# Optimization experiments

Measured on AMD Instinct MI355X. Metric: run time of the kernel, lower is better.

The kernel has to match this reference:

```python
import jax, jax.numpy as jnp
import numpy as np

B, L, D, H = 2, 2048, 1024, 16
DK = D // H


def setup_inputs() -> dict:
    key = jax.random.key(0)
    ks = jax.random.split(key, 11)
    s = 1.0 / np.sqrt(D)
    inp = {
        "context_sequence": jax.random.normal(ks[0], (B, L, D), jnp.float32),
        "value_sequence": jax.random.normal(ks[1], (B, L, D), jnp.float32),
        "mask": jnp.tril(jnp.ones((L, L), jnp.int32)),  # causal mask [L, L]
        "Wq": jax.random.normal(ks[2], (D, D), jnp.float32) * s,
        "bq": jax.random.normal(ks[3], (D,), jnp.float32) * s,
        "Wk": jax.random.normal(ks[4], (D, D), jnp.float32) * s,
        "bk": jax.random.normal(ks[5], (D,), jnp.float32) * s,
        "Wv": jax.random.normal(ks[6], (D, D), jnp.float32) * s,
        "bv": jax.random.normal(ks[7], (D,), jnp.float32) * s,
        "Wo": jax.random.normal(ks[8], (D, D), jnp.float32) * s,
        "bo": jax.random.normal(ks[9], (D,), jnp.float32) * s,
    }
    return inp


def reference(context_sequence, value_sequence, mask, Wq, bq, Wk, bk, Wv, bv, Wo, bo):
    orig_dtype = context_sequence.dtype
    # QKV projections; Q,K from context, V from value stream
    Q = (context_sequence @ Wq + bq).reshape(B, L, H, DK)
    K = (context_sequence @ Wk + bk).reshape(B, L, H, DK)
    V = (value_sequence @ Wv + bv).reshape(B, L, H, DK)
    # fp32 QK^T with 1/sqrt(d_k) scaling -> [B, H, L, L]
    scores = jnp.einsum("bqhd,bkhd->bhqk", Q.astype(jnp.float32), K.astype(jnp.float32)) / jnp.sqrt(
        jnp.asarray(DK, jnp.float32)
    )
    # dtype-dependent neg fill (fp32 -> -inf); causal rows always have >=1 valid entry
    neg_fill = jnp.asarray(-jnp.inf, jnp.float32)
    scores = jnp.where(mask[None, None, :, :] == 0, neg_fill, scores)
    scores = scores.astype(orig_dtype)
    attn = jax.nn.softmax(scores, axis=-1)
    # dropout is identity in eval mode
    out = jnp.einsum("bhqk,bkhd->bqhd", attn, V).reshape(B, L, D)
    return out @ Wo + bo
```

## Files before the change

### kernel.cpp

```cpp
#include <hip/hip_runtime.h>
#include <hip/hip_bf16.h>
#include <stdint.h>

#define B_   2
#define L_   2048
#define D_   1024
#define H_   16
#define DK_  64

typedef __attribute__((ext_vector_type(4))) float f32x4;
typedef __attribute__((ext_vector_type(8))) short short8;
typedef unsigned short ushort_t;

__device__ __forceinline__ ushort_t f2bf(float f) {
    union { float f; uint32_t u; } v; v.f = f;
    uint32_t r = v.u + 0x7FFFu + ((v.u >> 16) & 1u);
    return (ushort_t)(r >> 16);
}
__device__ __forceinline__ float bf2f(ushort_t u) {
    union { uint32_t u; float f; } v; v.u = (uint32_t)u << 16; return v.f;
}

__device__ __forceinline__ void async_copy16(void* lds, const void* g) {
    __builtin_amdgcn_global_load_lds(
        (const __attribute__((address_space(1))) uint32_t*)g,
        (__attribute__((address_space(3))) uint32_t*)lds, 16, 0, 0);
}

__global__ void cast_f32_bf16(const float* __restrict__ s0, const float* __restrict__ s1,
                              ushort_t* __restrict__ d0, ushort_t* __restrict__ d1) {
    const float* s = blockIdx.z ? s1 : s0;
    ushort_t*    d = blockIdx.z ? d1 : d0;
    int i = (blockIdx.x * 256 + threadIdx.x) * 4;
    float4 v = *(const float4*)(s + i);
    ushort4 o;
    o.x = f2bf(v.x); o.y = f2bf(v.y); o.z = f2bf(v.z); o.w = f2bf(v.w);
    *(ushort4*)(d + i) = o;
}

__global__ void transpose_w(const float* __restrict__ w0, const float* __restrict__ w1,
                            const float* __restrict__ w2, const float* __restrict__ w3,
                            ushort_t* __restrict__ out) {
    __shared__ float tile[32][33];
    const float* w = (blockIdx.z == 0) ? w0 : (blockIdx.z == 1) ? w1 : (blockIdx.z == 2) ? w2 : w3;
    ushort_t* o = out + (size_t)blockIdx.z * D_ * D_;
    int tx = threadIdx.x, ty = threadIdx.y;
    int k0 = blockIdx.y * 32, d0 = blockIdx.x * 32;
#pragma unroll
    for (int i = 0; i < 4; i++)
        tile[ty + i * 8][tx] = w[(size_t)(k0 + ty + i * 8) * D_ + d0 + tx];
    __syncthreads();
#pragma unroll
    for (int i = 0; i < 4; i++)
        o[(size_t)(d0 + ty + i * 8) * D_ + k0 + tx] = f2bf(tile[tx][ty + i * 8]);
}

__device__ __forceinline__ void gemm_main(const ushort_t* __restrict__ A,
                                          const ushort_t* __restrict__ WT,
                                          char* smem, int m0, int n0, int tid,
                                          f32x4 (&acc)[4][4]) {
    const int wid = tid >> 6, lane = tid & 63;
    const int wm = (wid >> 1) * 64, wn = (wid & 1) * 64;
#pragma unroll
    for (int i = 0; i < 4; i++)
#pragma unroll
        for (int j = 0; j < 4; j++) { f32x4 z = {0.f, 0.f, 0.f, 0.f}; acc[i][j] = z; }

    auto stage = [&](int buf, int k0) {
        char* bA = smem + buf * 32768;
        char* bB = bA + 16384;
#pragma unroll
        for (int i = 0; i < 4; i++) {
            int flat = i * 256 + tid; int row = flat >> 3; int win = (flat & 7) * 16;
            const char* srcA = (const char*)A + ((size_t)(m0 + row) * D_ + k0) * 2 + (win ^ ((row & 7) << 4));
            async_copy16(bA + (i * 256 + wid * 64) * 16, srcA);
            const char* srcB = (const char*)WT + ((size_t)(n0 + row) * D_ + k0) * 2 + (win ^ ((row & 7) << 4));
            async_copy16(bB + (i * 256 + wid * 64) * 16, srcB);
        }
    };

    stage(0, 0);
    int cur = 0;
    for (int k0 = 0; k0 < D_; k0 += 64) {
        __syncthreads();
        if (k0 + 64 < D_) stage(cur ^ 1, k0 + 64);
        const char* bA = smem + cur * 32768;
        const char* bB = bA + 16384;
#pragma unroll
        for (int ks = 0; ks < 2; ks++) {
            short8 af[4], bf[4];
            int kb = ks * 64 + ((lane >> 4) << 4);
#pragma unroll
            for (int t = 0; t < 4; t++) {
                int ml = wm + t * 16 + (lane & 15);
                af[t] = *(const short8*)(bA + ml * 128 + (kb ^ ((ml & 7) << 4)));
                int nl = wn + t * 16 + (lane & 15);
                bf[t] = *(const short8*)(bB + nl * 128 + (kb ^ ((nl & 7) << 4)));
            }
#pragma unroll
            for (int mt = 0; mt < 4; mt++)
#pragma unroll
                for (int nt = 0; nt < 4; nt++)
                    acc[mt][nt] = __builtin_amdgcn_mfma_f32_16x16x32_bf16(af[mt], bf[nt], acc[mt][nt], 0, 0, 0);
        }
        cur ^= 1;
    }
}

#define QSCALE 0.18033688f

__global__ __launch_bounds__(256, 2) void gemm_qkv(
    const ushort_t* __restrict__ Xc, const ushort_t* __restrict__ Xv,
    const ushort_t* __restrict__ WT0,
    const float* __restrict__ bq, const float* __restrict__ bk, const float* __restrict__ bv,
    ushort_t* __restrict__ qw, ushort_t* __restrict__ kw, ushort_t* __restrict__ vtw) {
    __shared__ __align__(16) char smem[65536];
    const int z = blockIdx.z;
    const ushort_t* A  = (z == 2) ? Xv : Xc;
    const ushort_t* WT = WT0 + (size_t)z * D_ * D_;
    const float* bias  = (z == 0) ? bq : (z == 1) ? bk : bv;
    const int tid = threadIdx.x, wid = tid >> 6, lane = tid & 63;
    const int m0 = blockIdx.y * 128, n0 = blockIdx.x * 128;
    const int wm = (wid >> 1) * 64, wn = (wid & 1) * 64;
    f32x4 acc[4][4];
    gemm_main(A, WT, smem, m0, n0, tid, acc);
#pragma unroll
    for (int mt = 0; mt < 4; mt++)
#pragma unroll
        for (int nt = 0; nt < 4; nt++)
#pragma unroll
            for (int r = 0; r < 4; r++) {
                int m = m0 + wm + mt * 16 + ((lane >> 4) << 2) + r;
                int n = n0 + wn + nt * 16 + (lane & 15);
                float v = acc[mt][nt][r] + bias[n];
                int b = m >> 11, tok = m & 2047, h = n >> 6, dk = n & 63;
                if (z == 0)      qw[((size_t)(b * H_ + h) * L_ + tok) * DK_ + dk] = f2bf(v * QSCALE);
                else if (z == 1) kw[((size_t)(b * H_ + h) * L_ + tok) * DK_ + dk] = f2bf(v);
                else             vtw[((size_t)(b * H_ + h) * DK_ + dk) * L_ + tok] = f2bf(v);
            }
}

__global__ __launch_bounds__(256, 2) void gemm_out(
    const ushort_t* __restrict__ O, const ushort_t* __restrict__ WT,
    const float* __restrict__ bo, float* __restrict__ out) {
    __shared__ __align__(16) char smem[65536];
    const int tid = threadIdx.x, wid = tid >> 6, lane = tid & 63;
    const int m0 = blockIdx.y * 128, n0 = blockIdx.x * 128;
    const int wm = (wid >> 1) * 64, wn = (wid & 1) * 64;
    f32x4 acc[4][4];
    gemm_main(O, WT, smem, m0, n0, tid, acc);
#pragma unroll
    for (int mt = 0; mt < 4; mt++)
#pragma unroll
        for (int nt = 0; nt < 4; nt++)
#pragma unroll
            for (int r = 0; r < 4; r++) {
                int m = m0 + wm + mt * 16 + ((lane >> 4) << 2) + r;
                int n = n0 + wn + nt * 16 + (lane & 15);
                out[(size_t)m * D_ + n] = acc[mt][nt][r] + bo[n];
            }
}

__global__ __launch_bounds__(256, 2) void attn_kernel(
    const ushort_t* __restrict__ qws, const ushort_t* __restrict__ kws,
    const ushort_t* __restrict__ vtws, ushort_t* __restrict__ ows) {
    __shared__ __align__(16) char smem[37888];
    const int tid = threadIdx.x, wid = tid >> 6, lane = tid & 63;
    const int lo = lane & 15, hi = lane >> 4;
    const int bid = blockIdx.x;
    const int xcd = bid & 7, slot = bid >> 3;
    const int bh = xcd * 4 + (slot >> 4);
    const int pi = slot & 15;
    char*  Pw = smem + wid * 9216;
    float* lw = (float*)(smem + 36864) + wid * 64;

    short8 ones;
#pragma unroll
    for (int i = 0; i < 8; i++) ones[i] = (short)0x3F80;

#pragma unroll 1
    for (int half = 0; half < 2; half++) {
        const int qtb = half ? (31 - pi) : pi;
        const int Q0 = qtb * 64;

        short8 qf[4][2];
#pragma unroll
        for (int qt = 0; qt < 4; qt++)
#pragma unroll
            for (int ks = 0; ks < 2; ks++)
                qf[qt][ks] = *(const short8*)(qws + (size_t)(bh * L_ + Q0 + qt * 16 + lo) * DK_ + ks * 32 + hi * 8);

        f32x4 oa[4][4];
        f32x4 lf4[4];
#pragma unroll
        for (int qt = 0; qt < 4; qt++) {
            f32x4 z = {0.f, 0.f, 0.f, 0.f};
            lf4[qt] = z;
#pragma unroll
            for (int ot = 0; ot < 4; ot++) oa[qt][ot] = z;
        }

        const int ntiles = qtb + 1;
#pragma unroll 1
        for (int t = wid; t < ntiles; t += 4) {
            const int k0 = t * 64;
            short8 vf[4][2];
#pragma unroll
            for (int ot = 0; ot < 4; ot++)
#pragma unroll
                for (int ks = 0; ks < 2; ks++)
                    vf[ot][ks] = *(const short8*)(vtws + (size_t)(bh * DK_ + ot * 16 + lo) * L_ + k0 + ks * 32 + hi * 8);

            const bool diag = (t == qtb);
#pragma unroll
            for (int kt = 0; kt < 4; kt++) {
                const ushort_t* krow = kws + (size_t)(bh * L_ + k0 + kt * 16 + lo) * DK_ + hi * 8;
                short8 kf0 = *(const short8*)(krow);
                short8 kf1 = *(const short8*)(krow + 32);
                f32x4 s[4];
#pragma unroll
                for (int qt = 0; qt < 4; qt++) {
                    f32x4 z = {0.f, 0.f, 0.f, 0.f};
                    s[qt] = __builtin_amdgcn_mfma_f32_16x16x32_bf16(qf[qt][0], kf0, z, 0, 0, 0);
                    s[qt] = __builtin_amdgcn_mfma_f32_16x16x32_bf16(qf[qt][1], kf1, s[qt], 0, 0, 0);
                }
                const int keyl = kt * 16 + lo;
#pragma unroll
                for (int qt = 0; qt < 4; qt++)
#pragma unroll
                    for (int r = 0; r < 4; r++) {
                        float p = exp2f(s[qt][r] - 32.f);
                        if (diag && (keyl > qt * 16 + 4 * hi + r)) p = 0.f;
                        *(ushort_t*)(Pw + (qt * 16 + 4 * hi + r) * 144 + keyl * 2) =
                            (ushort_t)(__float_as_uint(p) >> 16);
                    }
            }
            short8 pf[4][2];
#pragma unroll
            for (int qt = 0; qt < 4; qt++)
#pragma unroll
                for (int ks = 0; ks < 2; ks++)
                    pf[qt][ks] = *(const short8*)(Pw + (qt * 16 + lo) * 144 + ks * 64 + hi * 16);
#pragma unroll
            for (int ot = 0; ot < 4; ot++)
#pragma unroll
                for (int qt = 0; qt < 4; qt++) {
                    oa[qt][ot] = __builtin_amdgcn_mfma_f32_16x16x32_bf16(pf[qt][0], vf[ot][0], oa[qt][ot], 0, 0, 0);
                    oa[qt][ot] = __builtin_amdgcn_mfma_f32_16x16x32_bf16(pf[qt][1], vf[ot][1], oa[qt][ot], 0, 0, 0);
                }
#pragma unroll
            for (int qt = 0; qt < 4; qt++) {
                lf4[qt] = __builtin_amdgcn_mfma_f32_16x16x32_bf16(pf[qt][0], ones, lf4[qt], 0, 0, 0);
                lf4[qt] = __builtin_amdgcn_mfma_f32_16x16x32_bf16(pf[qt][1], ones, lf4[qt], 0, 0, 0);
            }
        }

#pragma unroll
        for (int qt = 0; qt < 4; qt++)
#pragma unroll
            for (int ot = 0; ot < 4; ot++)
#pragma unroll
                for (int r = 0; r < 4; r++)
                    *(ushort_t*)(Pw + (qt * 16 + 4 * hi + r) * 144 + (ot * 16 + lo) * 2) = f2bf(oa[qt][ot][r]);
        if (lo == 0) {
#pragma unroll
            for (int qt = 0; qt < 4; qt++)
                *(f32x4*)(lw + qt * 16 + 4 * hi) = lf4[qt];
        }
        __syncthreads();

        {
            const int q = tid >> 2, c = tid & 3;
            float acc[16];
#pragma unroll
            for (int j = 0; j < 16; j++) acc[j] = 0.f;
#pragma unroll
            for (int w = 0; w < 4; w++) {
                const char* base = smem + w * 9216 + q * 144 + c * 32;
                short8 a = *(const short8*)(base);
                short8 b = *(const short8*)(base + 16);
#pragma unroll
                for (int j = 0; j < 8; j++) acc[j]     += bf2f((ushort_t)a[j]);
#pragma unroll
                for (int j = 0; j < 8; j++) acc[8 + j] += bf2f((ushort_t)b[j]);
            }
            float ls = 0.f;
#pragma unroll
            for (int w = 0; w < 4; w++) ls += ((const float*)(smem + 36864))[w * 64 + q];
            float ri = 1.0f / ls;
            short8 o0, o1;
#pragma unroll
            for (int j = 0; j < 8; j++) o0[j] = (short)f2bf(acc[j] * ri);
#pragma unroll
            for (int j = 0; j < 8; j++) o1[j] = (short)f2bf(acc[8 + j] * ri);
            size_t ob = (size_t)((bh >> 4) * L_ + Q0 + q) * D_ + (bh & 15) * DK_ + c * 16;
            *(short8*)(ows + ob)     = o0;
            *(short8*)(ows + ob + 8) = o1;
        }
        __syncthreads();
    }
}

extern "C" void kernel_launch(void* const* d_in, const int* in_sizes, int n_in,
                              void* d_out, int out_size, void* d_ws, size_t ws_size,
                              hipStream_t stream) {
    (void)in_sizes; (void)n_in; (void)out_size; (void)ws_size;
    const float* ctx = (const float*)d_in[0];
    const float* val = (const float*)d_in[1];
    const float* Wq = (const float*)d_in[3];
    const float* bq = (const float*)d_in[4];
    const float* Wk = (const float*)d_in[5];
    const float* bk = (const float*)d_in[6];
    const float* Wv = (const float*)d_in[7];
    const float* bv = (const float*)d_in[8];
    const float* Wo = (const float*)d_in[9];
    const float* bo = (const float*)d_in[10];
    float* out = (float*)d_out;

    char* ws = (char*)d_ws;
    ushort_t* xc  = (ushort_t*)(ws);
    ushort_t* xv  = (ushort_t*)(ws + 8388608);
    ushort_t* wt  = (ushort_t*)(ws + 16777216);
    ushort_t* qws = (ushort_t*)(ws + 25165824);
    ushort_t* kws = (ushort_t*)(ws + 33554432);
    ushort_t* vtw = (ushort_t*)(ws + 41943040);

    cast_f32_bf16<<<dim3(4096, 1, 2), 256, 0, stream>>>(ctx, val, xc, xv);
    transpose_w<<<dim3(32, 32, 4), dim3(32, 8), 0, stream>>>(Wq, Wk, Wv, Wo, wt);
    gemm_qkv<<<dim3(8, 32, 3), 256, 0, stream>>>(xc, xv, wt, bq, bk, bv, qws, kws, vtw);
    attn_kernel<<<dim3(512), 256, 0, stream>>>(qws, kws, vtw, xc );
    gemm_out<<<dim3(8, 32), 256, 0, stream>>>(xc, wt + (size_t)3 * D_ * D_, bo, out);
}
```

Baseline: 129.0 us.

## One query tile per attention block, transposed QK MFMA with packed swizzled P stores

Each attention block now handles a single 64-row query tile, with blocks ordered heaviest-first, instead of a balanced pair of tiles. The grid doubles to 1024 blocks. QK^T is computed with K as the A operand so each lane holds four consecutive keys. Those are packed into bf16 pairs with perm and written as 8-byte XOR-swizzled LDS stores rather than scalar 2-byte stores. The -32 exponent offset is folded into the MFMA accumulator init, and P·V and the row-sum MFMAs are interleaved per k-slice. The aim is to cut LDS store count and bank conflicts and to improve scheduling, at the risk of load imbalance from the causal triangle without pairing.

```diff
diff --git a/kernel.cpp b/kernel.cpp
--- a/kernel.cpp
+++ b/kernel.cpp
@@ -168,136 +168,127 @@
     const int tid = threadIdx.x, wid = tid >> 6, lane = tid & 63;
     const int lo = lane & 15, hi = lane >> 4;
     const int bid = blockIdx.x;
-    const int xcd = bid & 7, slot = bid >> 3;
-    const int bh = xcd * 4 + (slot >> 4);
-    const int pi = slot & 15;
+    const int bh  = (bid & 7) * 4 + (bid >> 8);
+    const int qtb = 31 - ((bid >> 3) & 31);
+    const int Q0 = qtb * 64;
     char*  Pw = smem + wid * 9216;
     float* lw = (float*)(smem + 36864) + wid * 64;
+    const int swz = (lo & 7) << 4;
 
     short8 ones;
 #pragma unroll
     for (int i = 0; i < 8; i++) ones[i] = (short)0x3F80;
-
+    const f32x4 minit = {-32.f, -32.f, -32.f, -32.f};
+
+    short8 qf[4][2];
+#pragma unroll
+    for (int qt = 0; qt < 4; qt++)
+#pragma unroll
+        for (int ks = 0; ks < 2; ks++)
+            qf[qt][ks] = *(const short8*)(qws + (size_t)(bh * L_ + Q0 + qt * 16 + lo) * DK_ + ks * 32 + hi * 8);
+
+    f32x4 oa[4][4];
+    f32x4 lf4[4];
+#pragma unroll
+    for (int qt = 0; qt < 4; qt++) {
+        f32x4 z = {0.f, 0.f, 0.f, 0.f};
+        lf4[qt] = z;
+#pragma unroll
+        for (int ot = 0; ot < 4; ot++) oa[qt][ot] = z;
+    }
+
+    const int ntiles = qtb + 1;
 #pragma unroll 1
-    for (int half = 0; half < 2; half++) {
-        const int qtb = half ? (31 - pi) : pi;
-        const int Q0 = qtb * 64;
-
-        short8 qf[4][2];
+    for (int t = wid; t < ntiles; t += 4) {
+        const int k0 = t * 64;
+        const bool diag = (t == qtb);
+        short8 vf[4][2];
+#pragma unroll
+        for (int ot = 0; ot < 4; ot++)
+#pragma unroll
+            for (int ks = 0; ks < 2; ks++)
+                vf[ot][ks] = *(const short8*)(vtws + (size_t)(bh * DK_ + ot * 16 + lo) * L_ + k0 + ks * 32 + hi * 8);
+
+#pragma unroll
+        for (int kt = 0; kt < 4; kt++) {
+            const ushort_t* krow = kws + (size_t)(bh * L_ + k0 + kt * 16 + lo) * DK_ + hi * 8;
+            short8 kf0 = *(const short8*)(krow);
+            short8 kf1 = *(const short8*)(krow + 32);
+            const int kb = kt * 16 + 4 * hi;
+#pragma unroll
+            for (int qt = 0; qt < 4; qt++) {
+                f32x4 s = __builtin_amdgcn_mfma_f32_16x16x32_bf16(kf0, qf[qt][0], minit, 0, 0, 0);
+                s = __builtin_amdgcn_mfma_f32_16x16x32_bf16(kf1, qf[qt][1], s, 0, 0, 0);
+                float p0 = exp2f(s[0]);
+                float p1 = exp2f(s[1]);
+                float p2 = exp2f(s[2]);
+                float p3 = exp2f(s[3]);
+                if (diag) {
+                    const int qg = qt * 16 + lo;
+                    p0 = (kb > qg)     ? 0.f : p0;
+                    p1 = (kb + 1 > qg) ? 0.f : p1;
+                    p2 = (kb + 2 > qg) ? 0.f : p2;
+                    p3 = (kb + 3 > qg) ? 0.f : p3;
+                }
+                uint2 w;
+                w.x = __builtin_amdgcn_perm(__float_as_uint(p1), __float_as_uint(p0), 0x07060302u);
+                w.y = __builtin_amdgcn_perm(__float_as_uint(p3), __float_as_uint(p2), 0x07060302u);
+                *(uint2*)(Pw + qt * 2048 + lo * 128 + ((kt * 32 + hi * 8) ^ swz)) = w;
+            }
+        }
 #pragma unroll
         for (int qt = 0; qt < 4; qt++)
 #pragma unroll
-            for (int ks = 0; ks < 2; ks++)
-                qf[qt][ks] = *(const short8*)(qws + (size_t)(bh * L_ + Q0 + qt * 16 + lo) * DK_ + ks * 32 + hi * 8);
-
-        f32x4 oa[4][4];
-        f32x4 lf4[4];
-#pragma unroll
-        for (int qt = 0; qt < 4; qt++) {
-            f32x4 z = {0.f, 0.f, 0.f, 0.f};
-            lf4[qt] = z;
-#pragma unroll
-            for (int ot = 0; ot < 4; ot++) oa[qt][ot] = z;
+            for (int ks = 0; ks < 2; ks++) {
+                short8 pf = *(const short8*)(Pw + qt * 2048 + lo * 128 + ((ks * 64 + hi * 16) ^ swz));
+                lf4[qt] = __builtin_amdgcn_mfma_f32_16x16x32_bf16(pf, ones, lf4[qt], 0, 0, 0);
+#pragma unroll
+                for (int ot = 0; ot < 4; ot++)
+                    oa[qt][ot] = __builtin_amdgcn_mfma_f32_16x16x32_bf16(pf, vf[ot][ks], oa[qt][ot], 0, 0, 0);
+            }
+    }
+
+#pragma unroll
+    for (int qt = 0; qt < 4; qt++)
+#pragma unroll
+        for (int ot = 0; ot < 4; ot++)
+#pragma unroll
+            for (int r = 0; r < 4; r++)
+                *(ushort_t*)(Pw + (qt * 16 + 4 * hi + r) * 144 + (ot * 16 + lo) * 2) = f2bf(oa[qt][ot][r]);
+    if (lo == 0) {
+#pragma unroll
+        for (int qt = 0; qt < 4; qt++)
+            *(f32x4*)(lw + qt * 16 + 4 * hi) = lf4[qt];
+    }
+    __syncthreads();
+
+    {
+        const int q = tid >> 2, c = tid & 3;
+        float acc[16];
+#pragma unroll
+        for (int j = 0; j < 16; j++) acc[j] = 0.f;
+#pragma unroll
+        for (int w = 0; w < 4; w++) {
+            const char* base = smem + w * 9216 + q * 144 + c * 32;
+            short8 a = *(const short8*)(base);
+            short8 b = *(const short8*)(base + 16);
+#pragma unroll
+            for (int j = 0; j < 8; j++) acc[j]     += bf2f((ushort_t)a[j]);
+#pragma unroll
+            for (int j = 0; j < 8; j++) acc[8 + j] += bf2f((ushort_t)b[j]);
         }
-
-        const int ntiles = qtb + 1;
-#pragma unroll 1
-        for (int t = wid; t < ntiles; t += 4) {
-            const int k0 = t * 64;
-            short8 vf[4][2];
-#pragma unroll
-            for (int ot = 0; ot < 4; ot++)
-#pragma unroll
-                for (int ks = 0; ks < 2; ks++)
-                    vf[ot][ks] = *(const short8*)(vtws + (size_t)(bh * DK_ + ot * 16 + lo) * L_ + k0 + ks * 32 + hi * 8);
-
-            const bool diag = (t == qtb);
-#pragma unroll
-            for (int kt = 0; kt < 4; kt++) {
-                const ushort_t* krow = kws + (size_t)(bh * L_ + k0 + kt * 16 + lo) * DK_ + hi * 8;
-                short8 kf0 = *(const short8*)(krow);
-                short8 kf1 = *(const short8*)(krow + 32);
-                f32x4 s[4];
-#pragma unroll
-                for (int qt = 0; qt < 4; qt++) {
-                    f32x4 z = {0.f, 0.f, 0.f, 0.f};
-                    s[qt] = __builtin_amdgcn_mfma_f32_16x16x32_bf16(qf[qt][0], kf0, z, 0, 0, 0);
-                    s[qt] = __builtin_amdgcn_mfma_f32_16x16x32_bf16(qf[qt][1], kf1, s[qt], 0, 0, 0);
-                }
-                const int keyl = kt * 16 + lo;
-#pragma unroll
-                for (int qt = 0; qt < 4; qt++)
-#pragma unroll
-                    for (int r = 0; r < 4; r++) {
-                        float p = exp2f(s[qt][r] - 32.f);
-                        if (diag && (keyl > qt * 16 + 4 * hi + r)) p = 0.f;
-                        *(ushort_t*)(Pw + (qt * 16 + 4 * hi + r) * 144 + keyl * 2) =
-                            (ushort_t)(__float_as_uint(p) >> 16);
-                    }
-            }
-            short8 pf[4][2];
-#pragma unroll
-            for (int qt = 0; qt < 4; qt++)
-#pragma unroll
-                for (int ks = 0; ks < 2; ks++)
-                    pf[qt][ks] = *(const short8*)(Pw + (qt * 16 + lo) * 144 + ks * 64 + hi * 16);
-#pragma unroll
-            for (int ot = 0; ot < 4; ot++)
-#pragma unroll
-                for (int qt = 0; qt < 4; qt++) {
-                    oa[qt][ot] = __builtin_amdgcn_mfma_f32_16x16x32_bf16(pf[qt][0], vf[ot][0], oa[qt][ot], 0, 0, 0);
-                    oa[qt][ot] = __builtin_amdgcn_mfma_f32_16x16x32_bf16(pf[qt][1], vf[ot][1], oa[qt][ot], 0, 0, 0);
-                }
-#pragma unroll
-            for (int qt = 0; qt < 4; qt++) {
-                lf4[qt] = __builtin_amdgcn_mfma_f32_16x16x32_bf16(pf[qt][0], ones, lf4[qt], 0, 0, 0);
-                lf4[qt] = __builtin_amdgcn_mfma_f32_16x16x32_bf16(pf[qt][1], ones, lf4[qt], 0, 0, 0);
-            }
-        }
-
-#pragma unroll
-        for (int qt = 0; qt < 4; qt++)
-#pragma unroll
-            for (int ot = 0; ot < 4; ot++)
-#pragma unroll
-                for (int r = 0; r < 4; r++)
-                    *(ushort_t*)(Pw + (qt * 16 + 4 * hi + r) * 144 + (ot * 16 + lo) * 2) = f2bf(oa[qt][ot][r]);
-        if (lo == 0) {
-#pragma unroll
-            for (int qt = 0; qt < 4; qt++)
-                *(f32x4*)(lw + qt * 16 + 4 * hi) = lf4[qt];
-        }
-        __syncthreads();
-
-        {
-            const int q = tid >> 2, c = tid & 3;
-            float acc[16];
-#pragma unroll
-            for (int j = 0; j < 16; j++) acc[j] = 0.f;
-#pragma unroll
-            for (int w = 0; w < 4; w++) {
-                const char* base = smem + w * 9216 + q * 144 + c * 32;
-                short8 a = *(const short8*)(base);
-                short8 b = *(const short8*)(base + 16);
-#pragma unroll
-                for (int j = 0; j < 8; j++) acc[j]     += bf2f((ushort_t)a[j]);
-#pragma unroll
-                for (int j = 0; j < 8; j++) acc[8 + j] += bf2f((ushort_t)b[j]);
-            }
-            float ls = 0.f;
-#pragma unroll
-            for (int w = 0; w < 4; w++) ls += ((const float*)(smem + 36864))[w * 64 + q];
-            float ri = 1.0f / ls;
-            short8 o0, o1;
-#pragma unroll
-            for (int j = 0; j < 8; j++) o0[j] = (short)f2bf(acc[j] * ri);
-#pragma unroll
-            for (int j = 0; j < 8; j++) o1[j] = (short)f2bf(acc[8 + j] * ri);
-            size_t ob = (size_t)((bh >> 4) * L_ + Q0 + q) * D_ + (bh & 15) * DK_ + c * 16;
-            *(short8*)(ows + ob)     = o0;
-            *(short8*)(ows + ob + 8) = o1;
-        }
-        __syncthreads();
+        float ls = 0.f;
+#pragma unroll
+        for (int w = 0; w < 4; w++) ls += ((const float*)(smem + 36864))[w * 64 + q];
+        float ri = 1.0f / ls;
+        short8 o0, o1;
+#pragma unroll
+        for (int j = 0; j < 8; j++) o0[j] = (short)f2bf(acc[j] * ri);
+#pragma unroll
+        for (int j = 0; j < 8; j++) o1[j] = (short)f2bf(acc[8 + j] * ri);
+        size_t ob = (size_t)((bh >> 4) * L_ + Q0 + q) * D_ + (bh & 15) * DK_ + c * 16;
+        *(short8*)(ows + ob)     = o0;
+        *(short8*)(ows + ob + 8) = o1;
     }
 }
 
@@ -328,6 +319,6 @@
     cast_f32_bf16<<<dim3(4096, 1, 2), 256, 0, stream>>>(ctx, val, xc, xv);
     transpose_w<<<dim3(32, 32, 4), dim3(32, 8), 0, stream>>>(Wq, Wk, Wv, Wo, wt);
     gemm_qkv<<<dim3(8, 32, 3), 256, 0, stream>>>(xc, xv, wt, bq, bk, bv, qws, kws, vtw);
-    attn_kernel<<<dim3(512), 256, 0, stream>>>(qws, kws, vtw, xc );
+    attn_kernel<<<dim3(1024), 256, 0, stream>>>(qws, kws, vtw, xc );
     gemm_out<<<dim3(8, 32), 256, 0, stream>>>(xc, wt + (size_t)3 * D_ * D_, bo, out);
 }
```

Result: slower. 136.7 us (+5.9%).
